# Kernel tuning notes

Hardware: AMD Instinct MI355X
Metric: run time of the kernel (lower is better)

Reference implementation:

```python
import jax, jax.numpy as jnp
import numpy as np

B, N, M = 4, 4096, 4096
EPS = 1e-8
LOG_2PI = float(np.log(2.0 * 3.14159))  # module uses 3.14159, not math.pi


def setup_inputs() -> dict:
    key = jax.random.key(0)
    k1, k2, k3 = jax.random.split(key, 3)
    return {
        "pred_xyz": jax.random.normal(k1, (B, N, 3), dtype=jnp.float32),
        "pred_sigma": jax.random.uniform(k2, (B, N, 2), dtype=jnp.float32),
        "target": jax.random.normal(k3, (B, M, 3), dtype=jnp.float32),
    }


def reference(pred_xyz, pred_sigma, target):
    target_xyz = target[:, :, :3]
    # pairwise squared distances: [B, N, M]
    dist_xy = jnp.sum((pred_xyz[:, :, None, :2] - target_xyz[:, None, :, :2]) ** 2, axis=-1)
    dist_z = (pred_xyz[:, :, None, 2] - target_xyz[:, None, :, 2]) ** 2
    sigma_xy = pred_sigma[:, :, 0:1]  # [B, N, 1]
    sigma_z = pred_sigma[:, :, 1:2]   # [B, N, 1]
    log_coef = -jnp.log(sigma_xy + EPS) - 0.5 * jnp.log(sigma_z + EPS)  # [B, N, 1]
    log_probs = (log_coef - 1.5 * LOG_2PI
                 - 0.5 * dist_xy / (sigma_xy + EPS)
                 - 0.5 * dist_z / (sigma_z + EPS))  # [B, N, M]
    nll = -jax.nn.logsumexp(log_probs, axis=1)  # mixture over N predictions -> [B, M]
    return nll.mean()
```

## Files before the change

### kernel.cpp

```cpp
#include <hip/hip_runtime.h>


constexpr int Bc = 4, Nc = 4096, Mc = 4096;
constexpr int THREADS = 256;
constexpr int TM = 16;
constexpr int CHUNK = 512;
constexpr int NCHUNK = Nc / CHUNK;

#define EPS 1e-8f
constexpr float LOG2E   = 1.4426950408889634f;
constexpr float LN2     = 0.6931471805599453f;
constexpr float LOG_2PI = 1.8378762043478343f;
constexpr float K_CONST = -1.5f * LOG_2PI * LOG2E;

__global__ __launch_bounds__(THREADS, 4) void gmm_fused(
    const float* __restrict__ pred_xyz,
    const float* __restrict__ pred_sigma,
    const float* __restrict__ target,
    float* __restrict__ out)
{
    __shared__ float4 l4[2][CHUNK];
    __shared__ float2 l2[2][CHUNK];

    const int mt  = blockIdx.x;
    const int b   = blockIdx.y;
    const int tid = threadIdx.x;

    float tx[TM], ty[TM], tz[TM], txy2[TM], tz2[TM], acc[TM];
    const int m0 = mt * TM;
#pragma unroll
    for (int j = 0; j < TM; ++j) {
        const float* tp = target + ((size_t)b * Mc + m0 + j) * 3;
        tx[j] = tp[0]; ty[j] = tp[1]; tz[j] = tp[2];
        txy2[j] = tx[j] * tx[j] + ty[j] * ty[j];
        tz2[j]  = tz[j] * tz[j];
        acc[j]  = 0.f;
    }

    const float* pb = pred_xyz   + (size_t)b * Nc * 3;
    const float* sb = pred_sigma + (size_t)b * Nc * 2;

    for (int c = 0; c < NCHUNK; ++c) {
        const int buf = c & 1;
#pragma unroll
        for (int s = 0; s < 2; ++s) {
            const int nl = tid + s * THREADS;
            const int n  = c * CHUNK + nl;
            const float px = pb[n * 3], py = pb[n * 3 + 1], pz = pb[n * 3 + 2];
            const float sxy = sb[n * 2]     + EPS;
            const float sz  = sb[n * 2 + 1] + EPS;
            const float A  = -0.5f * LOG2E * __builtin_amdgcn_rcpf(sxy);
            const float C  = -0.5f * LOG2E * __builtin_amdgcn_rcpf(sz);
            const float k2 = -__builtin_amdgcn_logf(sxy)
                             - 0.5f * __builtin_amdgcn_logf(sz) + K_CONST;
            const float K2 = k2 + A * (px * px + py * py) + C * (pz * pz);
            l4[buf][nl] = make_float4(K2, A, C, -2.f * A * px);
            l2[buf][nl] = make_float2(-2.f * A * py, -2.f * C * pz);
        }
        __syncthreads();
#pragma unroll
        for (int s = 0; s < 2; ++s) {
            const int nl = tid + s * THREADS;
            const float4 r0 = l4[buf][nl];
            const float2 r1 = l2[buf][nl];
#pragma unroll
            for (int j = 0; j < TM; ++j) {
                float lp = fmaf(r0.y, txy2[j], r0.x);
                lp = fmaf(r0.z, tz2[j], lp);
                lp = fmaf(r0.w, tx[j], lp);
                lp = fmaf(r1.x, ty[j], lp);
                lp = fmaf(r1.y, tz[j], lp);
                acc[j] += __builtin_amdgcn_exp2f(lp);
            }
        }
    }

#pragma unroll
    for (int j = 0; j < TM; ++j) {
#pragma unroll
        for (int off = 32; off; off >>= 1)
            acc[j] += __shfl_down(acc[j], off, 64);
    }
    __syncthreads();
    float* red = (float*)&l4[0][0];
    const int wave = tid >> 6, lane = tid & 63;
    if (lane == 0) {
#pragma unroll
        for (int j = 0; j < TM; ++j) red[wave * TM + j] = acc[j];
    }
    __syncthreads();
    if (tid < TM) {
        const float s = red[tid] + red[TM + tid] + red[2 * TM + tid] + red[3 * TM + tid];
        float v = __builtin_amdgcn_logf(s);
#pragma unroll
        for (int off = 8; off; off >>= 1)
            v += __shfl_down(v, off, 64);
        if (tid == 0)
            atomicAdd(out, (-LN2 / (float)(Bc * Mc)) * v);
    }
}

extern "C" void kernel_launch(void* const* d_in, const int* in_sizes, int n_in,
                              void* d_out, int out_size, void* d_ws, size_t ws_size,
                              hipStream_t stream) {
    const float* pred_xyz   = (const float*)d_in[0];
    const float* pred_sigma = (const float*)d_in[1];
    const float* target     = (const float*)d_in[2];
    float* out = (float*)d_out;

    dim3 grid(Mc / TM, Bc);
    gmm_fused<<<grid, THREADS, 0, stream>>>(pred_xyz, pred_sigma, target, out);
}
```

Measured before the change: 79.18 us.

## Drop LDS staging and use packed FP32 FMAs over target pairs

Each thread now computes its own prediction coefficients directly from global memory instead of staging them through double-buffered shared memory with block-wide barriers. The per-target math is packed into 2-wide float vectors so the compiler can emit packed FP32 FMA instructions (v_pk_fma_f32) on CDNA. This removes LDS traffic and __syncthreads per chunk and halves the FMA instruction count. The exp2 calls stay scalar, so the transcendental unit may still be the limit.

```diff
diff --git a/kernel.cpp b/kernel.cpp
--- a/kernel.cpp
+++ b/kernel.cpp
@@ -4,8 +4,7 @@
 constexpr int Bc = 4, Nc = 4096, Mc = 4096;
 constexpr int THREADS = 256;
 constexpr int TM = 16;
-constexpr int CHUNK = 512;
-constexpr int NCHUNK = Nc / CHUNK;
+constexpr int PM = TM / 2;
 
 #define EPS 1e-8f
 constexpr float LOG2E   = 1.4426950408889634f;
@@ -13,80 +12,83 @@
 constexpr float LOG_2PI = 1.8378762043478343f;
 constexpr float K_CONST = -1.5f * LOG_2PI * LOG2E;
 
+typedef float v2f __attribute__((ext_vector_type(2)));
+
 __global__ __launch_bounds__(THREADS, 4) void gmm_fused(
     const float* __restrict__ pred_xyz,
     const float* __restrict__ pred_sigma,
     const float* __restrict__ target,
     float* __restrict__ out)
 {
-    __shared__ float4 l4[2][CHUNK];
-    __shared__ float2 l2[2][CHUNK];
-
     const int mt  = blockIdx.x;
     const int b   = blockIdx.y;
     const int tid = threadIdx.x;
 
-    float tx[TM], ty[TM], tz[TM], txy2[TM], tz2[TM], acc[TM];
+    v2f tx[PM], ty[PM], tz[PM], txy2[PM], tzz[PM], acc[PM];
     const int m0 = mt * TM;
 #pragma unroll
-    for (int j = 0; j < TM; ++j) {
-        const float* tp = target + ((size_t)b * Mc + m0 + j) * 3;
-        tx[j] = tp[0]; ty[j] = tp[1]; tz[j] = tp[2];
-        txy2[j] = tx[j] * tx[j] + ty[j] * ty[j];
-        tz2[j]  = tz[j] * tz[j];
-        acc[j]  = 0.f;
+    for (int p = 0; p < PM; ++p) {
+        const float* tp = target + ((size_t)b * Mc + m0 + 2 * p) * 3;
+        const float ax = tp[0], ay = tp[1], az = tp[2];
+        const float bx = tp[3], by = tp[4], bz = tp[5];
+        tx[p]   = (v2f){ax, bx};
+        ty[p]   = (v2f){ay, by};
+        tz[p]   = (v2f){az, bz};
+        txy2[p] = (v2f){ax * ax + ay * ay, bx * bx + by * by};
+        tzz[p]  = (v2f){az * az, bz * bz};
+        acc[p]  = (v2f){0.f, 0.f};
     }
 
-    const float* pb = pred_xyz   + (size_t)b * Nc * 3;
-    const float* sb = pred_sigma + (size_t)b * Nc * 2;
+    const float*  pb = pred_xyz + (size_t)b * Nc * 3;
+    const float2* sb = (const float2*)pred_sigma + (size_t)b * Nc;
 
-    for (int c = 0; c < NCHUNK; ++c) {
-        const int buf = c & 1;
+#pragma unroll 2
+    for (int n = tid; n < Nc; n += THREADS) {
+        const float px = pb[n * 3], py = pb[n * 3 + 1], pz = pb[n * 3 + 2];
+        const float2 s = sb[n];
+        const float sxy = s.x + EPS;
+        const float sz  = s.y + EPS;
+        const float A  = -0.5f * LOG2E * __builtin_amdgcn_rcpf(sxy);
+        const float C  = -0.5f * LOG2E * __builtin_amdgcn_rcpf(sz);
+        const float k2 = -__builtin_amdgcn_logf(sxy)
+                         - 0.5f * __builtin_amdgcn_logf(sz) + K_CONST;
+        const float K2 = k2 + A * (px * px + py * py) + C * (pz * pz);
+        const v2f vA  = (v2f){A, A};
+        const v2f vC  = (v2f){C, C};
+        const v2f vK  = (v2f){K2, K2};
+        const v2f vBx = (v2f){-2.f * A * px, -2.f * A * px};
+        const v2f vBy = (v2f){-2.f * A * py, -2.f * A * py};
+        const v2f vCz = (v2f){-2.f * C * pz, -2.f * C * pz};
 #pragma unroll
-        for (int s = 0; s < 2; ++s) {
-            const int nl = tid + s * THREADS;
-            const int n  = c * CHUNK + nl;
-            const float px = pb[n * 3], py = pb[n * 3 + 1], pz = pb[n * 3 + 2];
-            const float sxy = sb[n * 2]     + EPS;
-            const float sz  = sb[n * 2 + 1] + EPS;
-            const float A  = -0.5f * LOG2E * __builtin_amdgcn_rcpf(sxy);
-            const float C  = -0.5f * LOG2E * __builtin_amdgcn_rcpf(sz);
-            const float k2 = -__builtin_amdgcn_logf(sxy)
-                             - 0.5f * __builtin_amdgcn_logf(sz) + K_CONST;
-            const float K2 = k2 + A * (px * px + py * py) + C * (pz * pz);
-            l4[buf][nl] = make_float4(K2, A, C, -2.f * A * px);
-            l2[buf][nl] = make_float2(-2.f * A * py, -2.f * C * pz);
-        }
-        __syncthreads();
-#pragma unroll
-        for (int s = 0; s < 2; ++s) {
-            const int nl = tid + s * THREADS;
-            const float4 r0 = l4[buf][nl];
-            const float2 r1 = l2[buf][nl];
-#pragma unroll
-            for (int j = 0; j < TM; ++j) {
-                float lp = fmaf(r0.y, txy2[j], r0.x);
-                lp = fmaf(r0.z, tz2[j], lp);
-                lp = fmaf(r0.w, tx[j], lp);
-                lp = fmaf(r1.x, ty[j], lp);
-                lp = fmaf(r1.y, tz[j], lp);
-                acc[j] += __builtin_amdgcn_exp2f(lp);
-            }
+        for (int p = 0; p < PM; ++p) {
+            v2f t = __builtin_elementwise_fma(vA, txy2[p], vK);
+            t = __builtin_elementwise_fma(vC,  tzz[p], t);
+            t = __builtin_elementwise_fma(vBx, tx[p],  t);
+            t = __builtin_elementwise_fma(vBy, ty[p],  t);
+            t = __builtin_elementwise_fma(vCz, tz[p],  t);
+            v2f e;
+            e.x = __builtin_amdgcn_exp2f(t.x);
+            e.y = __builtin_amdgcn_exp2f(t.y);
+            acc[p] += e;
         }
     }
 
 #pragma unroll
-    for (int j = 0; j < TM; ++j) {
+    for (int p = 0; p < PM; ++p) {
 #pragma unroll
-        for (int off = 32; off; off >>= 1)
-            acc[j] += __shfl_down(acc[j], off, 64);
+        for (int off = 32; off; off >>= 1) {
+            acc[p].x += __shfl_down(acc[p].x, off, 64);
+            acc[p].y += __shfl_down(acc[p].y, off, 64);
+        }
     }
-    __syncthreads();
-    float* red = (float*)&l4[0][0];
+    __shared__ float red[4 * TM];
     const int wave = tid >> 6, lane = tid & 63;
     if (lane == 0) {
 #pragma unroll
-        for (int j = 0; j < TM; ++j) red[wave * TM + j] = acc[j];
+        for (int p = 0; p < PM; ++p) {
+            red[wave * TM + 2 * p]     = acc[p].x;
+            red[wave * TM + 2 * p + 1] = acc[p].y;
+        }
     }
     __syncthreads();
     if (tid < TM) {
```

Result: no change. 79.90 us (+0.9%).
